# Optimization experiments

Hardware: AMD Instinct MI355X
Metric: run time of the kernel (lower is better)

Reference implementation:

```python
import math
import jax, jax.numpy as jnp
import numpy as np

NUM_HEADS = 8
C_HIDDEN = 32
C_Q = 64
C_KV = 64
INF = 1.0e9


def setup_inputs() -> dict:
    key = jax.random.key(0)
    ks = jax.random.split(key, 8)
    B, S, Q, KV = 1, 128, 256, 256
    H, D = NUM_HEADS, C_HIDDEN
    input_q = jax.random.normal(ks[0], (B, S, Q, C_Q), dtype=jnp.float32)
    input_kv = jax.random.normal(ks[1], (B, S, KV, C_KV), dtype=jnp.float32)
    mask = jnp.ones((B, S, 1, 1, KV), dtype=jnp.float32)
    bias = jax.random.normal(ks[2], (B, 1, H, Q, KV), dtype=jnp.float32)
    # Glorot-ish init for projections
    wq = jax.random.normal(ks[3], (C_Q, H * D), dtype=jnp.float32) * (1.0 / math.sqrt(C_Q))
    wk = jax.random.normal(ks[4], (C_KV, H * D), dtype=jnp.float32) * (1.0 / math.sqrt(C_KV))
    wv = jax.random.normal(ks[5], (C_KV, H * D), dtype=jnp.float32) * (1.0 / math.sqrt(C_KV))
    wo = jax.random.normal(ks[6], (H * D, C_Q), dtype=jnp.float32) * (1.0 / math.sqrt(H * D))
    bo = jnp.zeros((C_Q,), dtype=jnp.float32)
    return {"input_q": input_q, "input_kv": input_kv, "mask": mask, "bias": bias,
            "wq": wq, "wk": wk, "wv": wv, "wo": wo, "bo": bo}


def _split_heads(x):
    # [..., L, H*D] -> [..., H, L, D]
    *lead, L, HD = x.shape
    x = x.reshape(*lead, L, NUM_HEADS, C_HIDDEN)
    return jnp.swapaxes(x, -2, -3)


def reference(input_q, input_kv, mask, bias, wq, wk, wv, wo, bo):
    q = _split_heads(input_q @ wq)   # [B,S,H,Q,D]
    k = _split_heads(input_kv @ wk)  # [B,S,H,KV,D]
    v = _split_heads(input_kv @ wv)  # [B,S,H,KV,D]
    scaling = 1.0 / math.sqrt(C_HIDDEN)
    a = jnp.einsum("bshqd,bshkd->bshqk", q * scaling, k)
    a = a + (mask - 1.0) * INF + bias
    a = jax.nn.softmax(a, axis=-1)
    o = jnp.einsum("bshqk,bshkd->bshqd", a, v)
    o = jnp.swapaxes(o, -2, -3)  # [B,S,Q,H,D]
    o = o.reshape(o.shape[:-2] + (NUM_HEADS * C_HIDDEN,))
    return o @ wo + bo
```

## Files before the change

### kernel.cpp

```cpp
#include <hip/hip_runtime.h>

typedef __bf16 bf16_t;
typedef __bf16 bf16x4_t __attribute__((ext_vector_type(4)));
typedef __bf16 bf16x8 __attribute__((ext_vector_type(8)));
typedef float f32x4 __attribute__((ext_vector_type(4)));

#define NH 8
#define DH 32
#define QL 256
#define KL 256
#define CIN 64
#define HD 256

__device__ __forceinline__ bf16_t f2bf(float x) { return (bf16_t)x; }

__device__ __forceinline__ f32x4 mfma16(bf16x8 a, bf16x8 b, f32x4 c) {
    return __builtin_amdgcn_mfma_f32_16x16x32_bf16(a, b, c, 0, 0, 0);
}

__launch_bounds__(256)
__global__ void pack_w(const float* __restrict__ Wq, const float* __restrict__ Wk,
                       const float* __restrict__ Wv, const float* __restrict__ Wo,
                       bf16_t* __restrict__ WqF, bf16_t* __restrict__ WkF,
                       bf16_t* __restrict__ WvF, bf16_t* __restrict__ WoF) {
    const int h = blockIdx.x;
    const int tid = threadIdx.x, lane = tid & 63, w = tid >> 6;
    const int quad = lane >> 4, l16 = lane & 15;
    if (w < 3) {
        const float* __restrict__ W = (w == 0) ? Wq : (w == 1 ? Wk : Wv);
        bf16_t* __restrict__ F = (w == 0) ? WqF : (w == 1 ? WkF : WvF);
#pragma unroll
        for (int nt = 0; nt < 2; ++nt)
#pragma unroll
            for (int ks = 0; ks < 2; ++ks) {
                bf16x8 f;
#pragma unroll
                for (int j = 0; j < 8; ++j)
                    f[j] = f2bf(W[(ks * 32 + quad * 8 + j) * HD + h * DH + nt * 16 + l16]);
                *(bf16x8*)&F[(size_t)((h * 4 + nt * 2 + ks) * 512) + lane * 8] = f;
            }
    } else {
#pragma unroll
        for (int nt = 0; nt < 4; ++nt) {
            bf16x8 f;
#pragma unroll
            for (int j = 0; j < 8; ++j)
                f[j] = f2bf(Wo[(h * DH + quad * 8 + j) * CIN + nt * 16 + l16]);
            *(bf16x8*)&WoF[(size_t)((h * 4 + nt) * 512) + lane * 8] = f;
        }
    }
}

__launch_bounds__(256, 2)
__global__ void fused_pipe(const float* __restrict__ Xq, const float* __restrict__ Xkv,
                           const float* __restrict__ Mask, const float* __restrict__ Bias,
                           const bf16_t* __restrict__ WqF, const bf16_t* __restrict__ WkF,
                           const bf16_t* __restrict__ WvF, const bf16_t* __restrict__ WoF,
                           const float* __restrict__ Bo, float* __restrict__ Out) {
    const int b = blockIdx.x;
    const int s = b & 127, qq = b >> 7;
    const int tid = threadIdx.x, lane = tid & 63, w = tid >> 6;
    const int quad = lane >> 4, l16 = lane & 15;
    const int tg = qq * 4 + w;
    const f32x4 vzero = {0.f, 0.f, 0.f, 0.f};

    __shared__ __attribute__((aligned(16))) bf16_t sK[2 * KL * 32];
    __shared__ __attribute__((aligned(16))) bf16_t sVT[2][DH][264];
    __shared__ __attribute__((aligned(16))) bf16_t sB[4][16][72];
    __shared__ __attribute__((aligned(16))) float sMask[KL];

    if (tid < 64) {
        const f32x4 m4 = *(const f32x4*)&Mask[s * KL + tid * 4];
        f32x4 mm;
#pragma unroll
        for (int j = 0; j < 4; ++j) mm[j] = (m4[j] - 1.0f) * 1.0e9f;
        *(f32x4*)&sMask[tid * 4] = mm;
    }

    bf16x8 xk[4][2];
#pragma unroll
    for (int t = 0; t < 4; ++t) {
        const int row = (w * 4 + t) * 16 + l16;
        const float* src = &Xkv[(size_t)(s * QL + row) * CIN];
#pragma unroll
        for (int ks = 0; ks < 2; ++ks) {
            const f32x4 lo = *(const f32x4*)&src[ks * 32 + quad * 8];
            const f32x4 hi = *(const f32x4*)&src[ks * 32 + quad * 8 + 4];
            bf16x8 f;
#pragma unroll
            for (int j = 0; j < 4; ++j) { f[j] = f2bf(lo[j]); f[4 + j] = f2bf(hi[j]); }
            xk[t][ks] = f;
        }
    }
    bf16x8 xq[2];
    {
        const int row = tg * 16 + l16;
        const float* src = &Xq[(size_t)(s * QL + row) * CIN];
#pragma unroll
        for (int ks = 0; ks < 2; ++ks) {
            const f32x4 lo = *(const f32x4*)&src[ks * 32 + quad * 8];
            const f32x4 hi = *(const f32x4*)&src[ks * 32 + quad * 8 + 4];
            bf16x8 f;
#pragma unroll
            for (int j = 0; j < 4; ++j) {
                f[j] = f2bf(lo[j] * 0.17677669529663687f);
                f[4 + j] = f2bf(hi[j] * 0.17677669529663687f);
            }
            xq[ks] = f;
        }
    }

    auto projKV = [&](int h, int buf) {
        bf16x8 bk[2][2], bv[2][2];
#pragma unroll
        for (int nt = 0; nt < 2; ++nt)
#pragma unroll
            for (int ks = 0; ks < 2; ++ks) {
                bk[nt][ks] = *(const bf16x8*)&WkF[(size_t)((h * 4 + nt * 2 + ks) * 512) + lane * 8];
                bv[nt][ks] = *(const bf16x8*)&WvF[(size_t)((h * 4 + nt * 2 + ks) * 512) + lane * 8];
            }
#pragma unroll
        for (int t = 0; t < 4; ++t) {
            const int r0 = (w * 4 + t) * 16 + quad * 4;
#pragma unroll
            for (int nt = 0; nt < 2; ++nt) {
                f32x4 c = mfma16(xk[t][0], bk[nt][0], vzero);
                c = mfma16(xk[t][1], bk[nt][1], c);
                const int chS = ((nt * 2 + (l16 >> 3)) ^ quad) << 3;
#pragma unroll
                for (int r = 0; r < 4; ++r)
                    sK[buf * (KL * 32) + (r0 + r) * 32 + chS + (l16 & 7)] = f2bf(c[r]);
            }
        }
#pragma unroll
        for (int t = 0; t < 4; ++t) {
            const int c0 = (w * 4 + t) * 16 + quad * 4;
#pragma unroll
            for (int nt = 0; nt < 2; ++nt) {
                f32x4 c = mfma16(xk[t][0], bv[nt][0], vzero);
                c = mfma16(xk[t][1], bv[nt][1], c);
                bf16x4_t p4;
#pragma unroll
                for (int r = 0; r < 4; ++r) p4[r] = f2bf(c[r]);
                *(bf16x4_t*)&sVT[buf][nt * 16 + l16][c0] = p4;
            }
        }
    };

    f32x4 acc[4];
#pragma unroll
    for (int nt = 0; nt < 4; ++nt) acc[nt] = vzero;

    projKV(0, 0);
    __syncthreads();

#pragma unroll 1
    for (int h = 0; h < NH; ++h) {
        const int p = h & 1;

        f32x4 sv[16];
        const float* bb = &Bias[(size_t)(h * QL + tg * 16 + l16) * KL];
#pragma unroll
        for (int ct = 0; ct < 16; ++ct) sv[ct] = *(const f32x4*)&bb[ct * 16 + quad * 4];

        bf16x8 qfr;
        {
            bf16x8 bq[2][2];
#pragma unroll
            for (int nt = 0; nt < 2; ++nt)
#pragma unroll
                for (int ks = 0; ks < 2; ++ks)
                    bq[nt][ks] = *(const bf16x8*)&WqF[(size_t)((h * 4 + nt * 2 + ks) * 512) + lane * 8];
#pragma unroll
            for (int nt = 0; nt < 2; ++nt) {
                f32x4 c = mfma16(xq[0], bq[nt][0], vzero);
                c = mfma16(xq[1], bq[nt][1], c);
#pragma unroll
                for (int r = 0; r < 4; ++r) sB[w][quad * 4 + r][nt * 16 + l16] = f2bf(c[r]);
            }
            qfr = *(const bf16x8*)&sB[w][l16][quad * 8];
        }

        bf16x8 bwo[4];
#pragma unroll
        for (int nt = 0; nt < 4; ++nt)
            bwo[nt] = *(const bf16x8*)&WoF[(size_t)((h * 4 + nt) * 512) + lane * 8];

        if (h + 1 < NH) projKV(h + 1, p ^ 1);

#pragma unroll
        for (int ct = 0; ct < 16; ++ct)
            sv[ct] += *(const f32x4*)&sMask[ct * 16 + quad * 4];
#pragma unroll
        for (int ct = 0; ct < 16; ++ct) {
            const int row = ct * 16 + l16;
            const int chS = (quad ^ ((l16 >> 2) & 3)) << 3;
            const bf16x8 ak = *(const bf16x8*)&sK[p * (KL * 32) + row * 32 + chS];
            sv[ct] = mfma16(ak, qfr, sv[ct]);
        }
        f32x4 vmx = sv[0];
#pragma unroll
        for (int ct = 1; ct < 16; ++ct)
#pragma unroll
            for (int r = 0; r < 4; ++r) vmx[r] = fmaxf(vmx[r], sv[ct][r]);
        float mx = fmaxf(fmaxf(vmx[0], vmx[1]), fmaxf(vmx[2], vmx[3]));
        mx = fmaxf(mx, __shfl_xor(mx, 16, 64));
        mx = fmaxf(mx, __shfl_xor(mx, 32, 64));
        f32x4 vsum = vzero;
#pragma unroll
        for (int ct = 0; ct < 16; ++ct)
#pragma unroll
            for (int r = 0; r < 4; ++r) {
                const float e = __expf(sv[ct][r] - mx);
                sv[ct][r] = e;
                vsum[r] += e;
            }
        float sum = (vsum[0] + vsum[1]) + (vsum[2] + vsum[3]);
        sum += __shfl_xor(sum, 16, 64);
        sum += __shfl_xor(sum, 32, 64);
        const float rs = 1.0f / sum;

        f32x4 o0 = vzero, o1 = vzero;
#pragma unroll
        for (int c = 0; c < 4; ++c) {
#pragma unroll
            for (int cc = 0; cc < 4; ++cc) {
                const int ct = c * 4 + cc;
                bf16x4_t pv;
#pragma unroll
                for (int r = 0; r < 4; ++r) pv[r] = f2bf(sv[ct][r] * rs);
                *(bf16x4_t*)&sB[w][l16][cc * 16 + quad * 4] = pv;
            }
#pragma unroll
            for (int ks = 0; ks < 2; ++ks) {
                const bf16x8 ap = *(const bf16x8*)&sB[w][l16][ks * 32 + quad * 8];
                const int cs = c * 2 + ks;
                const bf16x8 v0 = *(const bf16x8*)&sVT[p][l16][cs * 32 + quad * 8];
                const bf16x8 v1 = *(const bf16x8*)&sVT[p][16 + l16][cs * 32 + quad * 8];
                o0 = mfma16(ap, v0, o0);
                o1 = mfma16(ap, v1, o1);
            }
        }

        {
#pragma unroll
            for (int r = 0; r < 4; ++r) {
                sB[w][quad * 4 + r][l16] = f2bf(o0[r]);
                sB[w][quad * 4 + r][16 + l16] = f2bf(o1[r]);
            }
            const bf16x8 af = *(const bf16x8*)&sB[w][l16][quad * 8];
#pragma unroll
            for (int nt = 0; nt < 4; ++nt) acc[nt] = mfma16(af, bwo[nt], acc[nt]);
        }

        __syncthreads();
    }

    const int orow = s * QL + tg * 16 + quad * 4;
#pragma unroll
    for (int nt = 0; nt < 4; ++nt) {
        const float bo = Bo[nt * 16 + l16];
#pragma unroll
        for (int r = 0; r < 4; ++r)
            Out[(size_t)(orow + r) * CIN + nt * 16 + l16] = acc[nt][r] + bo;
    }
}

extern "C" void kernel_launch(void* const* d_in, const int* in_sizes, int n_in,
                              void* d_out, int out_size, void* d_ws, size_t ws_size,
                              hipStream_t stream) {
    const float* Xq   = (const float*)d_in[0];
    const float* Xkv  = (const float*)d_in[1];
    const float* Mask = (const float*)d_in[2];
    const float* Bias = (const float*)d_in[3];
    const float* Wq   = (const float*)d_in[4];
    const float* Wk   = (const float*)d_in[5];
    const float* Wv   = (const float*)d_in[6];
    const float* Wo   = (const float*)d_in[7];
    const float* Bo   = (const float*)d_in[8];
    float* Out = (float*)d_out;

    bf16_t* WqF = (bf16_t*)d_ws;
    bf16_t* WkF = WqF + 16384;
    bf16_t* WvF = WkF + 16384;
    bf16_t* WoF = WvF + 16384;

    pack_w<<<dim3(NH), 256, 0, stream>>>(Wq, Wk, Wv, Wo, WqF, WkF, WvF, WoF);
    fused_pipe<<<dim3(512), 256, 0, stream>>>(Xq, Xkv, Mask, Bias,
                                              WqF, WkF, WvF, WoF, Bo, Out);
}
```

Baseline: 131.0 us.

## Prefetch next-head bias and Q, swizzle LDS layouts, add MFMA priority hints

Bias for the next head is loaded into registers a full iteration ahead and used directly as the MFMA accumulator init. Q projection for the next head is computed at the end of the current iteration. The QK^T MFMAs now run before the next head's K/V projection. K is produced with swapped MFMA operands for vectorized 4-wide stores. The V^T, P and Q scratch buffers get XOR-swizzled, unpadded layouts to cut LDS bank conflicts, and s_setprio raises wave priority around MFMA bursts. This hides global bias latency and LDS conflicts at the cost of 64 extra live registers for the bias prefetch, which may pressure occupancy at 2 blocks/CU.

New measurement: 167.5 us. 27.9% more time.

```diff
diff --git a/kernel.cpp b/kernel.cpp
--- a/kernel.cpp
+++ b/kernel.cpp
@@ -52,11 +52,11 @@
 }
 
 __launch_bounds__(256, 2)
-__global__ void fused_pipe(const float* __restrict__ Xq, const float* __restrict__ Xkv,
-                           const float* __restrict__ Mask, const float* __restrict__ Bias,
-                           const bf16_t* __restrict__ WqF, const bf16_t* __restrict__ WkF,
-                           const bf16_t* __restrict__ WvF, const bf16_t* __restrict__ WoF,
-                           const float* __restrict__ Bo, float* __restrict__ Out) {
+__global__ void fused_pipe2(const float* __restrict__ Xq, const float* __restrict__ Xkv,
+                            const float* __restrict__ Mask, const float* __restrict__ Bias,
+                            const bf16_t* __restrict__ WqF, const bf16_t* __restrict__ WkF,
+                            const bf16_t* __restrict__ WvF, const bf16_t* __restrict__ WoF,
+                            const float* __restrict__ Bo, float* __restrict__ Out) {
     const int b = blockIdx.x;
     const int s = b & 127, qq = b >> 7;
     const int tid = threadIdx.x, lane = tid & 63, w = tid >> 6;
@@ -64,9 +64,9 @@
     const int tg = qq * 4 + w;
     const f32x4 vzero = {0.f, 0.f, 0.f, 0.f};
 
-    __shared__ __attribute__((aligned(16))) bf16_t sK[2 * KL * 32];
-    __shared__ __attribute__((aligned(16))) bf16_t sVT[2][DH][264];
-    __shared__ __attribute__((aligned(16))) bf16_t sB[4][16][72];
+    __shared__ __attribute__((aligned(16))) bf16_t sK[2][KL * 32];
+    __shared__ __attribute__((aligned(16))) bf16_t sVT[2][DH * 256];
+    __shared__ __attribute__((aligned(16))) bf16_t sPT[4][16 * 72];
     __shared__ __attribute__((aligned(16))) float sMask[KL];
 
     if (tid < 64) {
@@ -119,39 +119,72 @@
                 bk[nt][ks] = *(const bf16x8*)&WkF[(size_t)((h * 4 + nt * 2 + ks) * 512) + lane * 8];
                 bv[nt][ks] = *(const bf16x8*)&WvF[(size_t)((h * 4 + nt * 2 + ks) * 512) + lane * 8];
             }
+        const int rsw = (l16 >> 2) & 3;
 #pragma unroll
         for (int t = 0; t < 4; ++t) {
-            const int r0 = (w * 4 + t) * 16 + quad * 4;
+            const int kv = (w * 4 + t) * 16 + l16;
 #pragma unroll
             for (int nt = 0; nt < 2; ++nt) {
-                f32x4 c = mfma16(xk[t][0], bk[nt][0], vzero);
-                c = mfma16(xk[t][1], bk[nt][1], c);
-                const int chS = ((nt * 2 + (l16 >> 3)) ^ quad) << 3;
-#pragma unroll
-                for (int r = 0; r < 4; ++r)
-                    sK[buf * (KL * 32) + (r0 + r) * 32 + chS + (l16 & 7)] = f2bf(c[r]);
+                f32x4 c = mfma16(bk[nt][0], xk[t][0], vzero);
+                c = mfma16(bk[nt][1], xk[t][1], c);
+                bf16x4_t p;
+#pragma unroll
+                for (int r = 0; r < 4; ++r) p[r] = f2bf(c[r]);
+                const int ch = (nt * 2 + (quad >> 1)) ^ rsw;
+                *(bf16x4_t*)&sK[buf][kv * 32 + ch * 8 + (quad & 1) * 4] = p;
             }
         }
 #pragma unroll
         for (int t = 0; t < 4; ++t) {
-            const int c0 = (w * 4 + t) * 16 + quad * 4;
+            const int ch0 = (w * 4 + t) * 2 + (quad >> 1);
 #pragma unroll
             for (int nt = 0; nt < 2; ++nt) {
                 f32x4 c = mfma16(xk[t][0], bv[nt][0], vzero);
                 c = mfma16(xk[t][1], bv[nt][1], c);
-                bf16x4_t p4;
-#pragma unroll
-                for (int r = 0; r < 4; ++r) p4[r] = f2bf(c[r]);
-                *(bf16x4_t*)&sVT[buf][nt * 16 + l16][c0] = p4;
+                bf16x4_t p;
+#pragma unroll
+                for (int r = 0; r < 4; ++r) p[r] = f2bf(c[r]);
+                const int d = nt * 16 + l16;
+                const int ch = ch0 ^ (l16 & 7);
+                *(bf16x4_t*)&sVT[buf][d * 256 + ch * 8 + (quad & 1) * 4] = p;
             }
         }
     };
 
+    auto projQ = [&](int h) -> bf16x8 {
+        bf16x8 bq[2][2];
+#pragma unroll
+        for (int nt = 0; nt < 2; ++nt)
+#pragma unroll
+            for (int ks = 0; ks < 2; ++ks)
+                bq[nt][ks] = *(const bf16x8*)&WqF[(size_t)((h * 4 + nt * 2 + ks) * 512) + lane * 8];
+#pragma unroll
+        for (int nt = 0; nt < 2; ++nt) {
+            f32x4 c = mfma16(xq[0], bq[nt][0], vzero);
+            c = mfma16(xq[1], bq[nt][1], c);
+#pragma unroll
+            for (int r = 0; r < 4; ++r) {
+                const int row = quad * 4 + r;
+                const int col = nt * 16 + l16;
+                const int ch = (col >> 3) ^ (row & 7);
+                sPT[w][row * 72 + ch * 8 + (col & 7)] = f2bf(c[r]);
+            }
+        }
+        return *(const bf16x8*)&sPT[w][l16 * 72 + (quad ^ (l16 & 7)) * 8];
+    };
+
     f32x4 acc[4];
 #pragma unroll
     for (int nt = 0; nt < 4; ++nt) acc[nt] = vzero;
 
+    f32x4 bias[16];
+    {
+        const float* bb = &Bias[(size_t)(tg * 16 + l16) * KL];
+#pragma unroll
+        for (int ct = 0; ct < 16; ++ct) bias[ct] = *(const f32x4*)&bb[ct * 16 + quad * 4];
+    }
     projKV(0, 0);
+    bf16x8 qfr = projQ(0);
     __syncthreads();
 
 #pragma unroll 1
@@ -159,45 +192,32 @@
         const int p = h & 1;
 
         f32x4 sv[16];
-        const float* bb = &Bias[(size_t)(h * QL + tg * 16 + l16) * KL];
-#pragma unroll
-        for (int ct = 0; ct < 16; ++ct) sv[ct] = *(const f32x4*)&bb[ct * 16 + quad * 4];
-
-        bf16x8 qfr;
-        {
-            bf16x8 bq[2][2];
-#pragma unroll
-            for (int nt = 0; nt < 2; ++nt)
-#pragma unroll
-                for (int ks = 0; ks < 2; ++ks)
-                    bq[nt][ks] = *(const bf16x8*)&WqF[(size_t)((h * 4 + nt * 2 + ks) * 512) + lane * 8];
-#pragma unroll
-            for (int nt = 0; nt < 2; ++nt) {
-                f32x4 c = mfma16(xq[0], bq[nt][0], vzero);
-                c = mfma16(xq[1], bq[nt][1], c);
-#pragma unroll
-                for (int r = 0; r < 4; ++r) sB[w][quad * 4 + r][nt * 16 + l16] = f2bf(c[r]);
-            }
-            qfr = *(const bf16x8*)&sB[w][l16][quad * 8];
-        }
+        __builtin_amdgcn_s_setprio(1);
+#pragma unroll
+        for (int ct = 0; ct < 16; ++ct) {
+            const int row = ct * 16 + l16;
+            const int ch = quad ^ ((l16 >> 2) & 3);
+            const bf16x8 ak = *(const bf16x8*)&sK[p][row * 32 + ch * 8];
+            sv[ct] = mfma16(ak, qfr, bias[ct]);
+        }
+        __builtin_amdgcn_s_setprio(0);
+
+        if (h + 1 < NH) {
+            const float* bb = &Bias[(size_t)((h + 1) * QL + tg * 16 + l16) * KL];
+#pragma unroll
+            for (int ct = 0; ct < 16; ++ct) bias[ct] = *(const f32x4*)&bb[ct * 16 + quad * 4];
+        }
+
+        if (h + 1 < NH) projKV(h + 1, p ^ 1);
 
         bf16x8 bwo[4];
 #pragma unroll
         for (int nt = 0; nt < 4; ++nt)
             bwo[nt] = *(const bf16x8*)&WoF[(size_t)((h * 4 + nt) * 512) + lane * 8];
 
-        if (h + 1 < NH) projKV(h + 1, p ^ 1);
-
 #pragma unroll
         for (int ct = 0; ct < 16; ++ct)
             sv[ct] += *(const f32x4*)&sMask[ct * 16 + quad * 4];
-#pragma unroll
-        for (int ct = 0; ct < 16; ++ct) {
-            const int row = ct * 16 + l16;
-            const int chS = (quad ^ ((l16 >> 2) & 3)) << 3;
-            const bf16x8 ak = *(const bf16x8*)&sK[p * (KL * 32) + row * 32 + chS];
-            sv[ct] = mfma16(ak, qfr, sv[ct]);
-        }
         f32x4 vmx = sv[0];
 #pragma unroll
         for (int ct = 1; ct < 16; ++ct)
@@ -229,29 +249,39 @@
                 bf16x4_t pv;
 #pragma unroll
                 for (int r = 0; r < 4; ++r) pv[r] = f2bf(sv[ct][r] * rs);
-                *(bf16x4_t*)&sB[w][l16][cc * 16 + quad * 4] = pv;
-            }
+                const int ch = (cc * 2 + (quad >> 1)) ^ (l16 & 7);
+                *(bf16x4_t*)&sPT[w][l16 * 72 + ch * 8 + (quad & 1) * 4] = pv;
+            }
+            __builtin_amdgcn_s_setprio(1);
 #pragma unroll
             for (int ks = 0; ks < 2; ++ks) {
-                const bf16x8 ap = *(const bf16x8*)&sB[w][l16][ks * 32 + quad * 8];
+                const int ch = (ks * 4 + quad) ^ (l16 & 7);
+                const bf16x8 ap = *(const bf16x8*)&sPT[w][l16 * 72 + ch * 8];
                 const int cs = c * 2 + ks;
-                const bf16x8 v0 = *(const bf16x8*)&sVT[p][l16][cs * 32 + quad * 8];
-                const bf16x8 v1 = *(const bf16x8*)&sVT[p][16 + l16][cs * 32 + quad * 8];
+                const int chv = (cs * 4 + quad) ^ (l16 & 7);
+                const bf16x8 v0 = *(const bf16x8*)&sVT[p][l16 * 256 + chv * 8];
+                const bf16x8 v1 = *(const bf16x8*)&sVT[p][(16 + l16) * 256 + chv * 8];
                 o0 = mfma16(ap, v0, o0);
                 o1 = mfma16(ap, v1, o1);
             }
+            __builtin_amdgcn_s_setprio(0);
         }
 
         {
 #pragma unroll
             for (int r = 0; r < 4; ++r) {
-                sB[w][quad * 4 + r][l16] = f2bf(o0[r]);
-                sB[w][quad * 4 + r][16 + l16] = f2bf(o1[r]);
-            }
-            const bf16x8 af = *(const bf16x8*)&sB[w][l16][quad * 8];
+                const int row = quad * 4 + r;
+                const int ch0 = (l16 >> 3) ^ (row & 7);
+                const int ch1 = (2 + (l16 >> 3)) ^ (row & 7);
+                sPT[w][row * 72 + ch0 * 8 + (l16 & 7)] = f2bf(o0[r]);
+                sPT[w][row * 72 + ch1 * 8 + (l16 & 7)] = f2bf(o1[r]);
+            }
+            const bf16x8 af = *(const bf16x8*)&sPT[w][l16 * 72 + (quad ^ (l16 & 7)) * 8];
 #pragma unroll
             for (int nt = 0; nt < 4; ++nt) acc[nt] = mfma16(af, bwo[nt], acc[nt]);
         }
+
+        if (h + 1 < NH) qfr = projQ(h + 1);
 
         __syncthreads();
     }
@@ -286,6 +316,6 @@
     bf16_t* WoF = WvF + 16384;
 
     pack_w<<<dim3(NH), 256, 0, stream>>>(Wq, Wk, Wv, Wo, WqF, WkF, WvF, WoF);
-    fused_pipe<<<dim3(512), 256, 0, stream>>>(Xq, Xkv, Mask, Bias,
-                                              WqF, WkF, WvF, WoF, Bo, Out);
+    fused_pipe2<<<dim3(512), 256, 0, stream>>>(Xq, Xkv, Mask, Bias,
+                                               WqF, WkF, WvF, WoF, Bo, Out);
 }
```

## Compute PV transposed in registers, use exp2 softmax, prefetch next head's bias

Applied to the files above, without the earlier changes.

The PV product is now computed transposed, with V^T as the A operand and the probabilities as the B operand built directly from registers. This removes the LDS round-trips for P and for the attention output, and Wo is repacked to match the new output fragment layout. Softmax folds log2(e) into the Q scale, the bias and the mask so a raw v_exp_f32 can be used, and normalisation is deferred until after PV. The next head's bias load and Q projection are moved into the current iteration, after PV, to overlap global latency. This raises register pressure from keeping the bias tile live, and the raw exp instruction skips denormal handling.

Result: slower. 139.4 us (+6.4%).

```diff
diff --git a/kernel.cpp b/kernel.cpp
--- a/kernel.cpp
+++ b/kernel.cpp
@@ -16,6 +16,12 @@
 
 __device__ __forceinline__ f32x4 mfma16(bf16x8 a, bf16x8 b, f32x4 c) {
     return __builtin_amdgcn_mfma_f32_16x16x32_bf16(a, b, c, 0, 0, 0);
+}
+
+__device__ __forceinline__ float exp2_raw(float x) {
+    float r;
+    asm("v_exp_f32 %0, %1" : "=v"(r) : "v"(x));
+    return r;
 }
 
 __launch_bounds__(256)
@@ -45,35 +51,37 @@
             bf16x8 f;
 #pragma unroll
             for (int j = 0; j < 8; ++j)
-                f[j] = f2bf(Wo[(h * DH + quad * 8 + j) * CIN + nt * 16 + l16]);
+                f[j] = f2bf(Wo[(h * DH + (j >> 2) * 16 + quad * 4 + (j & 3)) * CIN +
+                               nt * 16 + l16]);
             *(bf16x8*)&WoF[(size_t)((h * 4 + nt) * 512) + lane * 8] = f;
         }
     }
 }
 
 __launch_bounds__(256, 2)
-__global__ void fused_pipe(const float* __restrict__ Xq, const float* __restrict__ Xkv,
-                           const float* __restrict__ Mask, const float* __restrict__ Bias,
-                           const bf16_t* __restrict__ WqF, const bf16_t* __restrict__ WkF,
-                           const bf16_t* __restrict__ WvF, const bf16_t* __restrict__ WoF,
-                           const float* __restrict__ Bo, float* __restrict__ Out) {
+__global__ void fused_pipe3(const float* __restrict__ Xq, const float* __restrict__ Xkv,
+                            const float* __restrict__ Mask, const float* __restrict__ Bias,
+                            const bf16_t* __restrict__ WqF, const bf16_t* __restrict__ WkF,
+                            const bf16_t* __restrict__ WvF, const bf16_t* __restrict__ WoF,
+                            const float* __restrict__ Bo, float* __restrict__ Out) {
     const int b = blockIdx.x;
     const int s = b & 127, qq = b >> 7;
     const int tid = threadIdx.x, lane = tid & 63, w = tid >> 6;
     const int quad = lane >> 4, l16 = lane & 15;
     const int tg = qq * 4 + w;
     const f32x4 vzero = {0.f, 0.f, 0.f, 0.f};
-
-    __shared__ __attribute__((aligned(16))) bf16_t sK[2 * KL * 32];
+    constexpr float L2E = 1.4426950408889634f;
+
+    __shared__ __attribute__((aligned(16))) bf16_t sK[2][KL * 32];
     __shared__ __attribute__((aligned(16))) bf16_t sVT[2][DH][264];
-    __shared__ __attribute__((aligned(16))) bf16_t sB[4][16][72];
+    __shared__ __attribute__((aligned(16))) bf16_t sPT[4][16][72];
     __shared__ __attribute__((aligned(16))) float sMask[KL];
 
     if (tid < 64) {
         const f32x4 m4 = *(const f32x4*)&Mask[s * KL + tid * 4];
         f32x4 mm;
 #pragma unroll
-        for (int j = 0; j < 4; ++j) mm[j] = (m4[j] - 1.0f) * 1.0e9f;
+        for (int j = 0; j < 4; ++j) mm[j] = (m4[j] - 1.0f) * (1.0e9f * L2E);
         *(f32x4*)&sMask[tid * 4] = mm;
     }
 
@@ -96,6 +104,7 @@
     {
         const int row = tg * 16 + l16;
         const float* src = &Xq[(size_t)(s * QL + row) * CIN];
+        const float qs = 0.17677669529663687f * L2E;
 #pragma unroll
         for (int ks = 0; ks < 2; ++ks) {
             const f32x4 lo = *(const f32x4*)&src[ks * 32 + quad * 8];
@@ -103,8 +112,8 @@
             bf16x8 f;
 #pragma unroll
             for (int j = 0; j < 4; ++j) {
-                f[j] = f2bf(lo[j] * 0.17677669529663687f);
-                f[4 + j] = f2bf(hi[j] * 0.17677669529663687f);
+                f[j] = f2bf(lo[j] * qs);
+                f[4 + j] = f2bf(hi[j] * qs);
             }
             xq[ks] = f;
         }
@@ -129,7 +138,7 @@
                 const int chS = ((nt * 2 + (l16 >> 3)) ^ quad) << 3;
 #pragma unroll
                 for (int r = 0; r < 4; ++r)
-                    sK[buf * (KL * 32) + (r0 + r) * 32 + chS + (l16 & 7)] = f2bf(c[r]);
+                    sK[buf][(r0 + r) * 32 + chS + (l16 & 7)] = f2bf(c[r]);
             }
         }
 #pragma unroll
@@ -146,58 +155,62 @@
             }
         }
     };
+    auto projQ = [&](int h) -> bf16x8 {
+        bf16x8 bq[2][2];
+#pragma unroll
+        for (int nt = 0; nt < 2; ++nt)
+#pragma unroll
+            for (int ks = 0; ks < 2; ++ks)
+                bq[nt][ks] = *(const bf16x8*)&WqF[(size_t)((h * 4 + nt * 2 + ks) * 512) + lane * 8];
+#pragma unroll
+        for (int nt = 0; nt < 2; ++nt) {
+            f32x4 c = mfma16(xq[0], bq[nt][0], vzero);
+            c = mfma16(xq[1], bq[nt][1], c);
+#pragma unroll
+            for (int r = 0; r < 4; ++r) sPT[w][quad * 4 + r][nt * 16 + l16] = f2bf(c[r]);
+        }
+        return *(const bf16x8*)&sPT[w][l16][quad * 8];
+    };
 
     f32x4 acc[4];
 #pragma unroll
     for (int nt = 0; nt < 4; ++nt) acc[nt] = vzero;
 
+    f32x4 sv[16];
+    {
+        const float* bb = &Bias[(size_t)(tg * 16 + l16) * KL];
+#pragma unroll
+        for (int ct = 0; ct < 16; ++ct) sv[ct] = *(const f32x4*)&bb[ct * 16 + quad * 4];
+    }
     projKV(0, 0);
+    bf16x8 qfr = projQ(0);
     __syncthreads();
+#pragma unroll
+    for (int ct = 0; ct < 16; ++ct) {
+        const f32x4 m4 = *(const f32x4*)&sMask[ct * 16 + quad * 4];
+#pragma unroll
+        for (int r = 0; r < 4; ++r) sv[ct][r] = sv[ct][r] * L2E + m4[r];
+    }
 
 #pragma unroll 1
     for (int h = 0; h < NH; ++h) {
         const int p = h & 1;
 
-        f32x4 sv[16];
-        const float* bb = &Bias[(size_t)(h * QL + tg * 16 + l16) * KL];
-#pragma unroll
-        for (int ct = 0; ct < 16; ++ct) sv[ct] = *(const f32x4*)&bb[ct * 16 + quad * 4];
-
-        bf16x8 qfr;
-        {
-            bf16x8 bq[2][2];
-#pragma unroll
-            for (int nt = 0; nt < 2; ++nt)
-#pragma unroll
-                for (int ks = 0; ks < 2; ++ks)
-                    bq[nt][ks] = *(const bf16x8*)&WqF[(size_t)((h * 4 + nt * 2 + ks) * 512) + lane * 8];
-#pragma unroll
-            for (int nt = 0; nt < 2; ++nt) {
-                f32x4 c = mfma16(xq[0], bq[nt][0], vzero);
-                c = mfma16(xq[1], bq[nt][1], c);
-#pragma unroll
-                for (int r = 0; r < 4; ++r) sB[w][quad * 4 + r][nt * 16 + l16] = f2bf(c[r]);
-            }
-            qfr = *(const bf16x8*)&sB[w][l16][quad * 8];
-        }
-
-        bf16x8 bwo[4];
-#pragma unroll
-        for (int nt = 0; nt < 4; ++nt)
-            bwo[nt] = *(const bf16x8*)&WoF[(size_t)((h * 4 + nt) * 512) + lane * 8];
-
-        if (h + 1 < NH) projKV(h + 1, p ^ 1);
-
-#pragma unroll
-        for (int ct = 0; ct < 16; ++ct)
-            sv[ct] += *(const f32x4*)&sMask[ct * 16 + quad * 4];
 #pragma unroll
         for (int ct = 0; ct < 16; ++ct) {
             const int row = ct * 16 + l16;
             const int chS = (quad ^ ((l16 >> 2) & 3)) << 3;
-            const bf16x8 ak = *(const bf16x8*)&sK[p * (KL * 32) + row * 32 + chS];
+            const bf16x8 ak = *(const bf16x8*)&sK[p][row * 32 + chS];
             sv[ct] = mfma16(ak, qfr, sv[ct]);
         }
+
+        if (h + 1 < NH) projKV(h + 1, p ^ 1);
+
+        bf16x8 bwo[4];
+#pragma unroll
+        for (int nt = 0; nt < 4; ++nt)
+            bwo[nt] = *(const bf16x8*)&WoF[(size_t)((h * 4 + nt) * 512) + lane * 8];
+
         f32x4 vmx = sv[0];
 #pragma unroll
         for (int ct = 1; ct < 16; ++ct)
@@ -211,7 +224,7 @@
         for (int ct = 0; ct < 16; ++ct)
 #pragma unroll
             for (int r = 0; r < 4; ++r) {
-                const float e = __expf(sv[ct][r] - mx);
+                const float e = exp2_raw(sv[ct][r] - mx);
                 sv[ct][r] = e;
                 vsum[r] += e;
             }
@@ -220,37 +233,56 @@
         sum += __shfl_xor(sum, 32, 64);
         const float rs = 1.0f / sum;
 
-        f32x4 o0 = vzero, o1 = vzero;
-#pragma unroll
-        for (int c = 0; c < 4; ++c) {
-#pragma unroll
-            for (int cc = 0; cc < 4; ++cc) {
-                const int ct = c * 4 + cc;
-                bf16x4_t pv;
-#pragma unroll
-                for (int r = 0; r < 4; ++r) pv[r] = f2bf(sv[ct][r] * rs);
-                *(bf16x4_t*)&sB[w][l16][cc * 16 + quad * 4] = pv;
-            }
-#pragma unroll
-            for (int ks = 0; ks < 2; ++ks) {
-                const bf16x8 ap = *(const bf16x8*)&sB[w][l16][ks * 32 + quad * 8];
-                const int cs = c * 2 + ks;
-                const bf16x8 v0 = *(const bf16x8*)&sVT[p][l16][cs * 32 + quad * 8];
-                const bf16x8 v1 = *(const bf16x8*)&sVT[p][16 + l16][cs * 32 + quad * 8];
-                o0 = mfma16(ap, v0, o0);
-                o1 = mfma16(ap, v1, o1);
-            }
+        f32x4 ot0 = vzero, ot1 = vzero;
+#pragma unroll
+        for (int c = 0; c < 8; ++c) {
+            bf16x8 pf;
+#pragma unroll
+            for (int j = 0; j < 4; ++j) {
+                pf[j] = f2bf(sv[2 * c][j]);
+                pf[4 + j] = f2bf(sv[2 * c + 1][j]);
+            }
+            const bf16x4_t a00 = *(const bf16x4_t*)&sVT[p][l16][c * 32 + quad * 4];
+            const bf16x4_t a01 = *(const bf16x4_t*)&sVT[p][l16][c * 32 + 16 + quad * 4];
+            const bf16x4_t a10 = *(const bf16x4_t*)&sVT[p][16 + l16][c * 32 + quad * 4];
+            const bf16x4_t a11 = *(const bf16x4_t*)&sVT[p][16 + l16][c * 32 + 16 + quad * 4];
+            bf16x8 va0, va1;
+#pragma unroll
+            for (int j = 0; j < 4; ++j) {
+                va0[j] = a00[j];
+                va0[4 + j] = a01[j];
+                va1[j] = a10[j];
+                va1[4 + j] = a11[j];
+            }
+            ot0 = mfma16(va0, pf, ot0);
+            ot1 = mfma16(va1, pf, ot1);
+        }
+
+        if (h + 1 < NH) {
+            const float* bb = &Bias[(size_t)((h + 1) * QL + tg * 16 + l16) * KL];
+#pragma unroll
+            for (int ct = 0; ct < 16; ++ct) sv[ct] = *(const f32x4*)&bb[ct * 16 + quad * 4];
         }
 
         {
+            bf16x8 af;
 #pragma unroll
             for (int r = 0; r < 4; ++r) {
-                sB[w][quad * 4 + r][l16] = f2bf(o0[r]);
-                sB[w][quad * 4 + r][16 + l16] = f2bf(o1[r]);
-            }
-            const bf16x8 af = *(const bf16x8*)&sB[w][l16][quad * 8];
+                af[r] = f2bf(ot0[r] * rs);
+                af[4 + r] = f2bf(ot1[r] * rs);
+            }
 #pragma unroll
             for (int nt = 0; nt < 4; ++nt) acc[nt] = mfma16(af, bwo[nt], acc[nt]);
+        }
+
+        if (h + 1 < NH) {
+            qfr = projQ(h + 1);
+#pragma unroll
+            for (int ct = 0; ct < 16; ++ct) {
+                const f32x4 m4 = *(const f32x4*)&sMask[ct * 16 + quad * 4];
+#pragma unroll
+                for (int r = 0; r < 4; ++r) sv[ct][r] = sv[ct][r] * L2E + m4[r];
+            }
         }
 
         __syncthreads();
@@ -286,6 +318,6 @@
     bf16_t* WoF = WvF + 16384;
 
     pack_w<<<dim3(NH), 256, 0, stream>>>(Wq, Wk, Wv, Wo, WqF, WkF, WvF, WoF);
-    fused_pipe<<<dim3(512), 256, 0, stream>>>(Xq, Xkv, Mask, Bias,
-                                              WqF, WkF, WvF, WoF, Bo, Out);
-}
+    fused_pipe3<<<dim3(512), 256, 0, stream>>>(Xq, Xkv, Mask, Bias,
+                                               WqF, WkF, WvF, WoF, Bo, Out);
+}
```
